# Optimization experiments

Measured on AMD Instinct MI355X. Metric: run time of the kernel, lower is better.

## Reference

```python
import jax, jax.numpy as jnp
import numpy as np

N = 50000
D_IN = 128
D_OUT = 128
EPS = 1e-5


def setup_inputs() -> dict:
    key = jax.random.key(0)
    ks = jax.random.split(key, 10)
    x = jax.random.normal(ks[0], (N, D_IN), dtype=jnp.float32)
    edge_index = jax.random.randint(ks[1], (2, 800000), 0, N, dtype=jnp.int64)
    s_in = 1.0 / np.sqrt(D_IN)
    s_out = 1.0 / np.sqrt(D_OUT)
    return {
        "x": x,
        "edge_index": edge_index,
        # SAGEConv 1: lin_l (on aggregated neighbors, with bias), lin_r (root, no bias)
        "w1_l": jax.random.uniform(ks[2], (D_OUT, D_IN), jnp.float32, -s_in, s_in),
        "b1_l": jnp.zeros((D_OUT,), jnp.float32),
        "w1_r": jax.random.uniform(ks[3], (D_OUT, D_IN), jnp.float32, -s_in, s_in),
        # SAGEConv 2
        "w2_l": jax.random.uniform(ks[4], (D_OUT, D_OUT), jnp.float32, -s_out, s_out),
        "b2_l": jnp.zeros((D_OUT,), jnp.float32),
        "w2_r": jax.random.uniform(ks[5], (D_OUT, D_OUT), jnp.float32, -s_out, s_out),
        # BatchNorm affine params
        "bn_gamma": jnp.ones((D_OUT,), jnp.float32),
        "bn_beta": jnp.zeros((D_OUT,), jnp.float32),
    }


def _sage_conv(x, src, dst, w_l, b_l, w_r):
    # mean aggregation of source-node features into target nodes
    msg = x[src]                                              # [E, D]
    agg = jax.ops.segment_sum(msg, dst, num_segments=N)       # [N, D]
    cnt = jax.ops.segment_sum(jnp.ones((src.shape[0],), x.dtype), dst, num_segments=N)
    mean = agg / jnp.maximum(cnt, 1.0)[:, None]
    return mean @ w_l.T + b_l + x @ w_r.T


def _batch_norm(x, gamma, beta):
    mu = jnp.mean(x, axis=0)
    var = jnp.mean(jnp.square(x - mu), axis=0)  # biased, as in torch BN training
    return (x - mu) * jax.lax.rsqrt(var + EPS) * gamma + beta


def reference(x, edge_index, w1_l, b1_l, w1_r, w2_l, b2_l, w2_r, bn_gamma, bn_beta):
    src, dst = edge_index[0], edge_index[1]
    h = _sage_conv(x, src, dst, w1_l, b1_l, w1_r)
    h = _batch_norm(h, bn_gamma, bn_beta)
    h = jax.nn.relu(h)
    out = _sage_conv(h, src, dst, w2_l, b2_l, w2_r)
    return out
```

## Files before the change

kernel.cpp:

```cpp
#include <hip/hip_runtime.h>

#define D 128
#define EPS 1e-5f
#define SCAN_CHUNK 2048

typedef unsigned int uint;
typedef __attribute__((ext_vector_type(4))) float f32x4;
typedef __attribute__((ext_vector_type(8))) short s16x8;

__device__ __forceinline__ uint pack_bf16(float a, float b)
{
    uint ua = __float_as_uint(a);
    uint ub = __float_as_uint(b);
    ua += 0x7FFFu + ((ua >> 16) & 1u);
    ub += 0x7FFFu + ((ub >> 16) & 1u);
    return (ua >> 16) | (ub & 0xFFFF0000u);
}
__device__ __forceinline__ float bf_lo(uint v) { return __uint_as_float(v << 16); }
__device__ __forceinline__ float bf_hi(uint v) { return __uint_as_float(v & 0xFFFF0000u); }

__global__ void prep_kernel(const float* __restrict__ x, uint* __restrict__ xb, int ncvt,
                            const float* __restrict__ w1l, const float* __restrict__ w1r,
                            const float* __restrict__ w2l, const float* __restrict__ w2r,
                            uint* __restrict__ wb1, uint* __restrict__ wb2)
{
    int idx = blockIdx.x * 256 + threadIdx.x;
    if (idx < ncvt) {
        float4 v = ((const float4*)x)[idx];
        uint2 o;
        o.x = pack_bf16(v.x, v.y);
        o.y = pack_bf16(v.z, v.w);
        ((uint2*)xb)[idx] = o;
    } else {
        int r = idx - ncvt;
        if (r < 8192) {
            int layer = r >> 12;
            int rem = r & 4095;
            int lane = rem & 63;
            int knt = rem >> 6;
            int kstep = knt >> 3, nt = knt & 7;
            int nn = nt * 16 + (lane & 15);
            int kbase = kstep * 32 + (lane >> 4) * 8;
            const float* wl = layer ? w2l : w1l;
            const float* wr = layer ? w2r : w1r;
            uint* wb = layer ? wb2 : wb1;
            float v[8];
#pragma unroll
            for (int j = 0; j < 8; j++) {
                int k = kbase + j;
                v[j] = (k < D) ? wl[nn * D + k] : wr[nn * D + (k - D)];
            }
            uint4 o;
            o.x = pack_bf16(v[0], v[1]);
            o.y = pack_bf16(v[2], v[3]);
            o.z = pack_bf16(v[4], v[5]);
            o.w = pack_bf16(v[6], v[7]);
            ((uint4*)wb)[(kstep * 8 + nt) * 64 + lane] = o;
        }
    }
}

__global__ void hist_kernel(const int* __restrict__ dst, int* __restrict__ deg, int E)
{
    int e = blockIdx.x * 256 + threadIdx.x;
    if (e < E) atomicAdd(&deg[dst[e]], 1);
}

__global__ __launch_bounds__(256) void scanA_kernel(const int* __restrict__ deg,
                                                    int* __restrict__ bsum, int n)
{
    __shared__ int red[256];
    int base = blockIdx.x * SCAN_CHUNK;
    int s = 0;
    for (int i = threadIdx.x; i < SCAN_CHUNK; i += 256) {
        int idx = base + i;
        if (idx < n) s += deg[idx];
    }
    red[threadIdx.x] = s;
    __syncthreads();
    for (int off = 128; off > 0; off >>= 1) {
        if (threadIdx.x < off) red[threadIdx.x] += red[threadIdx.x + off];
        __syncthreads();
    }
    if (threadIdx.x == 0) bsum[blockIdx.x] = red[0];
}

__global__ void scanB_kernel(int* __restrict__ bsum, int nb)
{
    int t = threadIdx.x;
    int v = (t < nb) ? bsum[t] : 0;
    for (int off = 1; off < 64; off <<= 1) {
        int u = __shfl_up(v, off);
        if (t >= off) v += u;
    }
    int ex = __shfl_up(v, 1);
    if (t == 0) ex = 0;
    if (t < nb) bsum[t] = ex;
}

__global__ __launch_bounds__(256) void scanC_kernel(const int* __restrict__ deg,
                                                    const int* __restrict__ bsum,
                                                    int* __restrict__ rowptr,
                                                    int* __restrict__ cursor, int n, int E)
{
    __shared__ int tsum[256];
    int t = threadIdx.x;
    int tb = blockIdx.x * SCAN_CHUNK + t * 8;
    int v[8];
    int s = 0;
#pragma unroll
    for (int k = 0; k < 8; k++) {
        int idx = tb + k;
        v[k] = (idx < n) ? deg[idx] : 0;
        s += v[k];
    }
    tsum[t] = s;
    __syncthreads();
    for (int off = 1; off < 256; off <<= 1) {
        int u = (t >= off) ? tsum[t - off] : 0;
        __syncthreads();
        tsum[t] += u;
        __syncthreads();
    }
    int run = bsum[blockIdx.x] + tsum[t] - s;
#pragma unroll
    for (int k = 0; k < 8; k++) {
        int idx = tb + k;
        if (idx < n) { rowptr[idx] = run; cursor[idx] = run; run += v[k]; }
    }
    if (blockIdx.x == 0 && t == 0) rowptr[n] = E;
}

__global__ void fill_kernel(const int* __restrict__ src, const int* __restrict__ dst,
                            int* __restrict__ cursor, int* __restrict__ col, int E)
{
    int e = blockIdx.x * 256 + threadIdx.x;
    if (e < E) {
        int p = atomicAdd(&cursor[dst[e]], 1);
        col[p] = src[e];
    }
}

template<bool BN>
__global__ __launch_bounds__(256) void agg_kernel(const int* __restrict__ rowptr,
                                                  const int* __restrict__ col,
                                                  const uint* __restrict__ featb,
                                                  const float* __restrict__ scsh,
                                                  uint* __restrict__ aggb, int n)
{
    int node = blockIdx.x * 4 + (threadIdx.x >> 6);
    if (node >= n) return;
    int lane = threadIdx.x & 63;
    int sub = lane >> 4, l16 = lane & 15;
    int r0 = rowptr[node], r1 = rowptr[node + 1];
    uint4* out4 = (uint4*)aggb;
    if (r0 == r1) {
        if (lane < 16) out4[(size_t)node * 16 + l16] = make_uint4(0, 0, 0, 0);
        return;
    }
    float sc[8], sh[8];
    if (BN) {
        float4 s0 = ((const float4*)scsh)[l16 * 2];
        float4 s1 = ((const float4*)scsh)[l16 * 2 + 1];
        float4 t0 = ((const float4*)scsh)[32 + l16 * 2];
        float4 t1 = ((const float4*)scsh)[32 + l16 * 2 + 1];
        sc[0] = s0.x; sc[1] = s0.y; sc[2] = s0.z; sc[3] = s0.w;
        sc[4] = s1.x; sc[5] = s1.y; sc[6] = s1.z; sc[7] = s1.w;
        sh[0] = t0.x; sh[1] = t0.y; sh[2] = t0.z; sh[3] = t0.w;
        sh[4] = t1.x; sh[5] = t1.y; sh[6] = t1.z; sh[7] = t1.w;
    }
    float acc[8] = {0.f, 0.f, 0.f, 0.f, 0.f, 0.f, 0.f, 0.f};
    const uint4* fb = (const uint4*)featb;

    auto accum = [&](uint4 v) {
        float e[8] = {bf_lo(v.x), bf_hi(v.x), bf_lo(v.y), bf_hi(v.y),
                      bf_lo(v.z), bf_hi(v.z), bf_lo(v.w), bf_hi(v.w)};
#pragma unroll
        for (int j = 0; j < 8; j++) {
            float t = e[j];
            if (BN) t = fmaxf(t * sc[j] + sh[j], 0.f);
            acc[j] += t;
        }
    };

    int i = r0;
    for (; i + 16 <= r1; i += 16) {
        int c0 = col[i + sub], c1 = col[i + 4 + sub];
        int c2 = col[i + 8 + sub], c3 = col[i + 12 + sub];
        uint4 v0 = fb[(size_t)c0 * 16 + l16];
        uint4 v1 = fb[(size_t)c1 * 16 + l16];
        uint4 v2 = fb[(size_t)c2 * 16 + l16];
        uint4 v3 = fb[(size_t)c3 * 16 + l16];
        accum(v0); accum(v1); accum(v2); accum(v3);
    }
    for (; i < r1; i += 4) {
        int idx = i + sub;
        if (idx < r1) {
            uint4 v = fb[(size_t)col[idx] * 16 + l16];
            accum(v);
        }
    }
#pragma unroll
    for (int j = 0; j < 8; j++) {
        acc[j] += __shfl_down(acc[j], 32);
        acc[j] += __shfl_down(acc[j], 16);
    }
    if (lane < 16) {
        float inv = 1.0f / (float)(r1 - r0);
        uint4 o;
        o.x = pack_bf16(acc[0] * inv, acc[1] * inv);
        o.y = pack_bf16(acc[2] * inv, acc[3] * inv);
        o.z = pack_bf16(acc[4] * inv, acc[5] * inv);
        o.w = pack_bf16(acc[6] * inv, acc[7] * inv);
        out4[(size_t)node * 16 + l16] = o;
    }
}

#define TSTRIDE 132
template<bool FUSE1, bool BNP2>
__global__ __launch_bounds__(256) void conv_kernel(
    const uint* __restrict__ p1b, const uint* __restrict__ p2b,
    const uint* __restrict__ wb, const float* __restrict__ bias,
    const float* __restrict__ scsh, float* __restrict__ outf,
    uint* __restrict__ outb, float* __restrict__ pstats, int n)
{
    extern __shared__ float smem[];
    float* tile = smem;
    float* scs = smem;
    int w = threadIdx.x >> 6, lane = threadIdx.x & 63;
    int quad = lane >> 4, l15 = lane & 15;
    int nb = blockIdx.x * 64;

    if (BNP2) {
        scs[threadIdx.x] = scsh[threadIdx.x];
        __syncthreads();
    }

    const uint4* p1 = (const uint4*)p1b;
    const uint4* p2 = (const uint4*)p2b;
    const uint4* wv = (const uint4*)wb;

    uint4 B[8][2];
    int nt0 = w * 2;
#pragma unroll
    for (int ks = 0; ks < 8; ks++) {
#pragma unroll
        for (int t = 0; t < 2; t++)
            B[ks][t] = wv[(ks * 8 + nt0 + t) * 64 + lane];
    }

    float bv0 = bias[nt0 * 16 + l15];
    float bv1 = bias[nt0 * 16 + 16 + l15];

    for (int rt = 0; rt < 4; rt++) {
        int node = nb + rt * 16 + l15;
        int nc = min(node, n - 1);
        uint4 A[8];
#pragma unroll
        for (int ks = 0; ks < 4; ks++) A[ks] = p1[(size_t)nc * 16 + ks * 4 + quad];
#pragma unroll
        for (int ks = 0; ks < 4; ks++) A[ks + 4] = p2[(size_t)nc * 16 + ks * 4 + quad];

        if (BNP2) {
#pragma unroll
            for (int ks = 4; ks < 8; ks++) {
                int c0 = (ks - 4) * 32 + quad * 8;
                uint4 u = A[ks];
                float e[8] = {bf_lo(u.x), bf_hi(u.x), bf_lo(u.y), bf_hi(u.y),
                              bf_lo(u.z), bf_hi(u.z), bf_lo(u.w), bf_hi(u.w)};
#pragma unroll
                for (int j = 0; j < 8; j++)
                    e[j] = fmaxf(e[j] * scs[c0 + j] + scs[128 + c0 + j], 0.f);
                u.x = pack_bf16(e[0], e[1]);
                u.y = pack_bf16(e[2], e[3]);
                u.z = pack_bf16(e[4], e[5]);
                u.w = pack_bf16(e[6], e[7]);
                A[ks] = u;
            }
        }

        f32x4 acc0 = {bv0, bv0, bv0, bv0};
        f32x4 acc1 = {bv1, bv1, bv1, bv1};
#pragma unroll
        for (int ks = 0; ks < 8; ks++) {
            s16x8 a = *(s16x8*)&A[ks];
            acc0 = __builtin_amdgcn_mfma_f32_16x16x32_bf16(a, *(s16x8*)&B[ks][0], acc0, 0, 0, 0);
            acc1 = __builtin_amdgcn_mfma_f32_16x16x32_bf16(a, *(s16x8*)&B[ks][1], acc1, 0, 0, 0);
        }
        int row0 = nb + rt * 16 + quad * 4;
        int colbase = nt0 * 16 + l15;
        if (FUSE1) {
            int rloc0 = rt * 16 + quad * 4;
#pragma unroll
            for (int reg = 0; reg < 4; reg++) {
                bool ok = (row0 + reg) < n;
                tile[(rloc0 + reg) * TSTRIDE + colbase]      = ok ? acc0[reg] : 0.f;
                tile[(rloc0 + reg) * TSTRIDE + colbase + 16] = ok ? acc1[reg] : 0.f;
            }
        } else {
#pragma unroll
            for (int reg = 0; reg < 4; reg++) {
                int row = row0 + reg;
                if (row < n) {
                    outf[(size_t)row * D + colbase] = acc0[reg];
                    outf[(size_t)row * D + colbase + 16] = acc1[reg];
                }
            }
        }
    }

    if (FUSE1) {
        __syncthreads();
        int colj = threadIdx.x & 127, half = threadIdx.x >> 7;
        float s = 0.f, ss = 0.f;
        for (int r = half * 32; r < half * 32 + 32; r++) {
            float v = tile[r * TSTRIDE + colj];
            s += v;
            ss += v * v;
        }
        float* pb = pstats + (size_t)blockIdx.x * 512 + half * 256;
        pb[colj] = s;
        pb[128 + colj] = ss;
        uint4* ob4 = (uint4*)outb;
#pragma unroll
        for (int q4 = 0; q4 < 4; q4++) {
            int idx = q4 * 256 + threadIdx.x;
            int r = idx >> 4, q = idx & 15;
            int row = nb + r;
            if (row < n) {
                float* tr = &tile[r * TSTRIDE + q * 8];
                uint4 o;
                o.x = pack_bf16(tr[0], tr[1]);
                o.y = pack_bf16(tr[2], tr[3]);
                o.z = pack_bf16(tr[4], tr[5]);
                o.w = pack_bf16(tr[6], tr[7]);
                ob4[(size_t)row * 16 + q] = o;
            }
        }
    }
}

__global__ __launch_bounds__(256) void reduce_kernel(const float* __restrict__ pstats,
                                                     float* __restrict__ stats, int nparts)
{
    int j = threadIdx.x;
    int chunk = (nparts + gridDim.x - 1) / gridDim.x;
    int p0 = blockIdx.x * chunk;
    int p1 = min(p0 + chunk, nparts);
    float s = 0.f;
    for (int p = p0; p < p1; p++) s += pstats[(size_t)p * 256 + j];
    unsafeAtomicAdd(&stats[j], s);
}

__global__ void bnfin_kernel(const float* __restrict__ stats, const float* __restrict__ gamma,
                             const float* __restrict__ beta, float* __restrict__ scsh, float n_inv)
{
    int j = threadIdx.x;
    float mean = stats[j] * n_inv;
    float var = fmaxf(stats[128 + j] * n_inv - mean * mean, 0.f);
    float sc = gamma[j] * rsqrtf(var + EPS);
    scsh[j] = sc;
    scsh[128 + j] = beta[j] - mean * sc;
}

extern "C" void kernel_launch(void* const* d_in, const int* in_sizes, int n_in,
                              void* d_out, int out_size, void* d_ws, size_t ws_size,
                              hipStream_t stream)
{
    const float* x     = (const float*)d_in[0];
    const int*   ei    = (const int*)d_in[1];
    const float* w1_l  = (const float*)d_in[2];
    const float* b1_l  = (const float*)d_in[3];
    const float* w1_r  = (const float*)d_in[4];
    const float* w2_l  = (const float*)d_in[5];
    const float* b2_l  = (const float*)d_in[6];
    const float* w2_r  = (const float*)d_in[7];
    const float* gamma = (const float*)d_in[8];
    const float* beta  = (const float*)d_in[9];

    int N = in_sizes[0] / D;
    int E = in_sizes[1] / 2;
    const int* src = ei;
    const int* dst = ei + E;

    int cblocks = (N + 63) / 64;

    uint*  aggb   = (uint*)d_ws;
    uint*  xb     = aggb + (size_t)N * 64;
    uint*  hb     = xb + (size_t)N * 64;
    uint*  wb1    = hb + (size_t)N * 64;
    uint*  wb2    = wb1 + 16384;
    float* stats  = (float*)(wb2 + 16384);
    float* scsh   = stats + 256;
    float* pstats = scsh + 256;
    int*   deg    = (int*)(pstats + (size_t)cblocks * 512);
    int*   rowptr = deg + N;
    int*   cursor = rowptr + N + 1;
    int*   col    = cursor + N;
    int*   bsum   = col + E;

    hipMemsetAsync(deg, 0, (size_t)N * sizeof(int), stream);
    hipMemsetAsync(stats, 0, 256 * sizeof(float), stream);

    int ncvt = N * 32;
    int pblocks = (ncvt + 8192 + 255) / 256;
    prep_kernel<<<pblocks, 256, 0, stream>>>(x, xb, ncvt, w1_l, w1_r, w2_l, w2_r, wb1, wb2);

    int eblocks = (E + 255) / 256;
    int ablocks = (N + 3) / 4;
    int nscan   = (N + SCAN_CHUNK - 1) / SCAN_CHUNK;

    hist_kernel<<<eblocks, 256, 0, stream>>>(dst, deg, E);
    scanA_kernel<<<nscan, 256, 0, stream>>>(deg, bsum, N);
    scanB_kernel<<<1, 64, 0, stream>>>(bsum, nscan);
    scanC_kernel<<<nscan, 256, 0, stream>>>(deg, bsum, rowptr, cursor, N, E);
    fill_kernel<<<eblocks, 256, 0, stream>>>(src, dst, cursor, col, E);

    agg_kernel<false><<<ablocks, 256, 0, stream>>>(rowptr, col, xb, nullptr, aggb, N);
    conv_kernel<true, false><<<cblocks, 256, 64 * TSTRIDE * 4, stream>>>(
        aggb, xb, wb1, b1_l, nullptr, nullptr, hb, pstats, N);

    reduce_kernel<<<32, 256, 0, stream>>>(pstats, stats, cblocks * 2);
    bnfin_kernel<<<1, 128, 0, stream>>>(stats, gamma, beta, scsh, 1.0f / (float)N);

    agg_kernel<true><<<ablocks, 256, 0, stream>>>(rowptr, col, hb, scsh, aggb, N);
    conv_kernel<false, true><<<cblocks, 256, 256 * 4, stream>>>(
        aggb, hb, wb2, b2_l, scsh, (float*)d_out, nullptr, nullptr, N);
}
```

Baseline: 310.4 us.

## Replace global-atomic CSR fill with two-pass bucketed scatter

```diff
diff --git a/kernel.cpp b/kernel.cpp
--- a/kernel.cpp
+++ b/kernel.cpp
@@ -3,6 +3,7 @@
 #define D 128
 #define EPS 1e-5f
 #define SCAN_CHUNK 2048
+#define FB_EPB 8
 
 typedef unsigned int uint;
 typedef __attribute__((ext_vector_type(4))) float f32x4;
@@ -101,7 +102,7 @@
 __global__ __launch_bounds__(256) void scanC_kernel(const int* __restrict__ deg,
                                                     const int* __restrict__ bsum,
                                                     int* __restrict__ rowptr,
-                                                    int* __restrict__ cursor, int n, int E)
+                                                    int* __restrict__ bcur, int n, int E)
 {
     __shared__ int tsum[256];
     int t = threadIdx.x;
@@ -126,18 +127,65 @@
 #pragma unroll
     for (int k = 0; k < 8; k++) {
         int idx = tb + k;
-        if (idx < n) { rowptr[idx] = run; cursor[idx] = run; run += v[k]; }
+        if (idx < n) {
+            rowptr[idx] = run;
+            if ((idx & 511) == 0) bcur[(idx >> 9) * 16] = run;
+            run += v[k];
+        }
     }
     if (blockIdx.x == 0 && t == 0) rowptr[n] = E;
 }
 
-__global__ void fill_kernel(const int* __restrict__ src, const int* __restrict__ dst,
-                            int* __restrict__ cursor, int* __restrict__ col, int E)
-{
-    int e = blockIdx.x * 256 + threadIdx.x;
-    if (e < E) {
-        int p = atomicAdd(&cursor[dst[e]], 1);
-        col[p] = src[e];
+__global__ __launch_bounds__(512) void bfill_kernel(const int* __restrict__ src,
+                                                    const int* __restrict__ dst,
+                                                    int* __restrict__ bcur,
+                                                    uint2* __restrict__ ebuf,
+                                                    int E, int nbuck)
+{
+    __shared__ int cnt[128], base[128];
+    int t = threadIdx.x;
+    if (t < 128) cnt[t] = 0;
+    __syncthreads();
+    int e0 = blockIdx.x * (512 * FB_EPB);
+    int s[FB_EPB], d[FB_EPB], loc[FB_EPB];
+#pragma unroll
+    for (int k = 0; k < FB_EPB; k++) {
+        int e = e0 + k * 512 + t;
+        if (e < E) {
+            s[k] = src[e];
+            d[k] = dst[e];
+            loc[k] = atomicAdd(&cnt[d[k] >> 9], 1);
+        }
+    }
+    __syncthreads();
+    if (t < nbuck) base[t] = atomicAdd(&bcur[t * 16], cnt[t]);
+    __syncthreads();
+#pragma unroll
+    for (int k = 0; k < FB_EPB; k++) {
+        int e = e0 + k * 512 + t;
+        if (e < E) {
+            int b = d[k] >> 9;
+            ebuf[base[b] + loc[k]] = make_uint2((uint)s[k], (uint)d[k]);
+        }
+    }
+}
+
+__global__ __launch_bounds__(512) void pfill_kernel(const int* __restrict__ rowptr,
+                                                    const uint2* __restrict__ ebuf,
+                                                    int* __restrict__ col, int n)
+{
+    __shared__ int lcur[512];
+    int t = threadIdx.x;
+    int nb = blockIdx.x << 9;
+    int ncnt = min(512, n - nb);
+    if (t < ncnt) lcur[t] = rowptr[nb + t];
+    __syncthreads();
+    int e0 = rowptr[nb];
+    int e1 = rowptr[min(nb + 512, n)];
+    for (int i = e0 + t; i < e1; i += 512) {
+        uint2 ed = ebuf[i];
+        int p = atomicAdd(&lcur[(int)ed.y - nb], 1);
+        col[p] = (int)ed.x;
     }
 }
 
@@ -384,20 +432,22 @@
     const int* dst = ei + E;
 
     int cblocks = (N + 63) / 64;
+    int nbuck   = (N + 511) >> 9;
 
     uint*  aggb   = (uint*)d_ws;
     uint*  xb     = aggb + (size_t)N * 64;
     uint*  hb     = xb + (size_t)N * 64;
     uint*  wb1    = hb + (size_t)N * 64;
     uint*  wb2    = wb1 + 16384;
-    float* stats  = (float*)(wb2 + 16384);
+    uint2* ebuf   = (uint2*)(wb2 + 16384);
+    float* stats  = (float*)(ebuf + E);
     float* scsh   = stats + 256;
     float* pstats = scsh + 256;
     int*   deg    = (int*)(pstats + (size_t)cblocks * 512);
     int*   rowptr = deg + N;
-    int*   cursor = rowptr + N + 1;
-    int*   col    = cursor + N;
+    int*   col    = rowptr + N + 1;
     int*   bsum   = col + E;
+    int*   bcur   = bsum + 64;
 
     hipMemsetAsync(deg, 0, (size_t)N * sizeof(int), stream);
     hipMemsetAsync(stats, 0, 256 * sizeof(float), stream);
@@ -406,15 +456,17 @@
     int pblocks = (ncvt + 8192 + 255) / 256;
     prep_kernel<<<pblocks, 256, 0, stream>>>(x, xb, ncvt, w1_l, w1_r, w2_l, w2_r, wb1, wb2);
 
-    int eblocks = (E + 255) / 256;
-    int ablocks = (N + 3) / 4;
-    int nscan   = (N + SCAN_CHUNK - 1) / SCAN_CHUNK;
+    int eblocks  = (E + 255) / 256;
+    int ablocks  = (N + 3) / 4;
+    int bfblocks = (E + 4095) / 4096;
+    int nscan    = (N + SCAN_CHUNK - 1) / SCAN_CHUNK;
 
     hist_kernel<<<eblocks, 256, 0, stream>>>(dst, deg, E);
     scanA_kernel<<<nscan, 256, 0, stream>>>(deg, bsum, N);
     scanB_kernel<<<1, 64, 0, stream>>>(bsum, nscan);
-    scanC_kernel<<<nscan, 256, 0, stream>>>(deg, bsum, rowptr, cursor, N, E);
-    fill_kernel<<<eblocks, 256, 0, stream>>>(src, dst, cursor, col, E);
+    scanC_kernel<<<nscan, 256, 0, stream>>>(deg, bsum, rowptr, bcur, N, E);
+    bfill_kernel<<<bfblocks, 512, 0, stream>>>(src, dst, bcur, ebuf, E, nbuck);
+    pfill_kernel<<<nbuck, 512, 0, stream>>>(rowptr, ebuf, col, N);
 
     agg_kernel<false><<<ablocks, 256, 0, stream>>>(rowptr, col, xb, nullptr, aggb, N);
     conv_kernel<true, false><<<cblocks, 256, 64 * TSTRIDE * 4, stream>>>(
```

New measurement: 289.5 us. 6.7% less time.
